# Optimization experiments

Hardware: AMD Instinct MI355X
Metric: run time of the kernel (lower is better)

Reference implementation:

```python
import jax, jax.numpy as jnp
import numpy as np

DIM = 768
HID = 3072  # 4 * DIM
EPS = 1e-5


def layer_norm(x, w, b):
    mu = jnp.mean(x, axis=-1, keepdims=True)
    var = jnp.var(x, axis=-1, keepdims=True)
    return (x - mu) * jax.lax.rsqrt(var + EPS) * w + b


def setup_inputs() -> dict:
    key = jax.random.key(0)
    ks = jax.random.split(key, 8)
    C, H = DIM, HID
    s = lambda fan_in: 1.0 / np.sqrt(fan_in)
    return {
        "x": jax.random.normal(ks[0], (32, 577, C), dtype=jnp.float32),
        "norm1_w": jnp.ones((C,), jnp.float32),
        "norm1_b": jnp.zeros((C,), jnp.float32),
        "qkv_w": jax.random.uniform(ks[1], (3 * C, C), jnp.float32, -s(C), s(C)),
        "proj_w": jax.random.uniform(ks[2], (C, C), jnp.float32, -s(C), s(C)),
        "proj_b": jax.random.uniform(ks[3], (C,), jnp.float32, -s(C), s(C)),
        "norm2_w": jnp.ones((C,), jnp.float32),
        "norm2_b": jnp.zeros((C,), jnp.float32),
        "fc1_w": jax.random.uniform(ks[4], (H, C), jnp.float32, -s(C), s(C)),
        "fc1_b": jax.random.uniform(ks[5], (H,), jnp.float32, -s(C), s(C)),
        "fc2_w": jax.random.uniform(ks[6], (C, H), jnp.float32, -s(H), s(H)),
        "fc2_b": jax.random.uniform(ks[7], (C,), jnp.float32, -s(H), s(H)),
    }


def reference(x, norm1_w, norm1_b, qkv_w, proj_w, proj_b,
              norm2_w, norm2_b, fc1_w, fc1_b, fc2_w, fc2_b):
    B, N, C = x.shape
    attn_size = int((N - 1) ** 0.5)
    scale = C ** -0.5

    # --- Attention on norm1(x) (single head) ---
    h = layer_norm(x, norm1_w, norm1_b)
    qkv = (h @ qkv_w.T).reshape(B, N, 3, C)           # [B,N,3,C]
    q, k, v = qkv[:, :, 0], qkv[:, :, 1], qkv[:, :, 2]
    attn = jax.nn.softmax(jnp.einsum('bnc,bmc->bnm', q, k) * scale, axis=-1)
    y = jnp.einsum('bnm,bmc->bnc', attn, v)           # [B,N,C]
    # Faithful to torch: .transpose(1,2).reshape(B,N,C) scrambles layout
    y = jnp.transpose(y, (0, 2, 1)).reshape(B, N, C)
    a = y @ proj_w.T + proj_b
    token_attn = attn[:, 0, 1:].reshape(B, 1, attn_size, attn_size)

    # Faithful to torch Block: input residual is discarded, attention out doubled
    x = a + a

    # --- MLP (exact GELU, as nn.GELU default) ---
    m = layer_norm(x, norm2_w, norm2_b)
    m = jax.nn.gelu(m @ fc1_w.T + fc1_b, approximate=False)
    m = m @ fc2_w.T + fc2_b
    x = x + m
    return (x, token_attn)
```

## Files before the change

### kernel.cpp

```cpp
#include <hip/hip_runtime.h>
#include <hip/hip_bf16.h>

#define Bz   32
#define Nn_  577
#define Np   640
#define Cc   768
#define Hh   3072
#define Mrows (Bz * Nn_)
#define OUT_X (Mrows * Cc)
#define SCALE 0.03608439182435161f

typedef unsigned short ushort_t;
typedef short short8 __attribute__((ext_vector_type(8)));
typedef float f32x4 __attribute__((ext_vector_type(4)));

__device__ __forceinline__ ushort_t f2b(float f) {
    __hip_bfloat16 h = __float2bfloat16(f);
    return *reinterpret_cast<ushort_t*>(&h);
}

__device__ __forceinline__ void gl16(const ushort_t* g, ushort_t* l) {
    __builtin_amdgcn_global_load_lds(
        (const __attribute__((address_space(1))) void*)g,
        (__attribute__((address_space(3))) void*)l, 16, 0, 0);
}

__device__ __forceinline__ float bsum(float v, float* sm) {
    #pragma unroll
    for (int o = 32; o > 0; o >>= 1) v += __shfl_down(v, o, 64);
    int lane = threadIdx.x & 63, wid = threadIdx.x >> 6;
    if (lane == 0) sm[wid] = v;
    __syncthreads();
    float r = sm[0] + sm[1] + sm[2] + sm[3];
    __syncthreads();
    return r;
}
__device__ __forceinline__ float bmax(float v, float* sm) {
    #pragma unroll
    for (int o = 32; o > 0; o >>= 1) v = fmaxf(v, __shfl_down(v, o, 64));
    int lane = threadIdx.x & 63, wid = threadIdx.x >> 6;
    if (lane == 0) sm[wid] = v;
    __syncthreads();
    float r = fmaxf(fmaxf(sm[0], sm[1]), fmaxf(sm[2], sm[3]));
    __syncthreads();
    return r;
}

__global__ void cvt_kernel(const float* __restrict__ in, ushort_t* __restrict__ out, int n) {
    int i = blockIdx.x * 256 + threadIdx.x;
    if (i < n) out[i] = f2b(in[i]);
}

__global__ void ln_bf16(const float* __restrict__ x, const float* __restrict__ w,
                        const float* __restrict__ b, ushort_t* __restrict__ out) {
    __shared__ float sm[8];
    long long row = blockIdx.x;
    const float* xr = x + row * Cc;
    float v[3]; float s = 0.f;
    #pragma unroll
    for (int i = 0; i < 3; ++i) { v[i] = xr[threadIdx.x + i * 256]; s += v[i]; }
    float mu = bsum(s, sm) * (1.f / (float)Cc);
    float sq = 0.f;
    #pragma unroll
    for (int i = 0; i < 3; ++i) { float d = v[i] - mu; sq += d * d; }
    float var = bsum(sq, sm + 4) * (1.f / (float)Cc);
    float inv = rsqrtf(var + 1e-5f);
    ushort_t* orow = out + row * Cc;
    #pragma unroll
    for (int i = 0; i < 3; ++i) {
        int c = threadIdx.x + i * 256;
        orow[c] = f2b((v[i] - mu) * inv * w[c] + b[c]);
    }
}

__global__ void softmax_bf16(const float* __restrict__ Sf, ushort_t* __restrict__ Sb,
                             float* __restrict__ tok) {
    __shared__ float sm[8];
    long long row = blockIdx.x;
    int b_l = (int)(row / Nn_), r = (int)(row - (long long)b_l * Nn_);
    const float* src = Sf + row * Np;
    ushort_t* dst = Sb + row * Np;
    float v[3]; float mx = -1e30f;
    #pragma unroll
    for (int i = 0; i < 3; ++i) {
        int c = threadIdx.x + i * 256;
        v[i] = (c < Nn_) ? src[c] : -1e30f;
        mx = fmaxf(mx, v[i]);
    }
    mx = bmax(mx, sm);
    float s = 0.f;
    #pragma unroll
    for (int i = 0; i < 3; ++i) {
        int c = threadIdx.x + i * 256;
        v[i] = (c < Nn_) ? expf(v[i] - mx) : 0.f;
        s += v[i];
    }
    s = bsum(s, sm + 4);
    float inv = 1.f / s;
    #pragma unroll
    for (int i = 0; i < 3; ++i) {
        int c = threadIdx.x + i * 256;
        float p = v[i] * inv;
        if (c < Np) dst[c] = (c < Nn_) ? f2b(p) : (ushort_t)0;
        if (r == 0 && c >= 1 && c < Nn_) tok[(long long)b_l * 576 + (c - 1)] = p;
    }
}

#define EPS_STORE  0
#define EPS_X2     1
#define EPS_GELU   2
#define EPS_ATOMIC 3
#define EPS_QKV    4

template<int EPI, typename OutT>
__global__ __launch_bounds__(256)
void mm_bf16(const ushort_t* __restrict__ A, long long sAb, int lda, int M,
             const ushort_t* __restrict__ B, long long sBb, int ldb, int Nv,
             const float* __restrict__ bias,
             OutT* __restrict__ O, long long sOb, int ldo,
             int K, float alpha,
             ushort_t* __restrict__ qQ, ushort_t* __restrict__ qK, ushort_t* __restrict__ qV)
{
    __shared__ __align__(16) ushort_t As[128 * 32];
    __shared__ __align__(16) ushort_t Bs[128 * 32];
    const int z = blockIdx.z;
    A += (long long)z * sAb; B += (long long)z * sBb;
    if (O) O += (long long)z * sOb;
    const int n0 = blockIdx.x * 128;
    const int m0 = blockIdx.y * 128;
    const int tid = threadIdx.x;
    const int lane = tid & 63;
    const int wv = tid >> 6;
    const int wr = (wv >> 1) << 6;
    const int wc = (wv & 1) << 6;
    const int fr = lane & 15;
    const int kq = lane >> 4;

    const int e0 = tid * 8, e1 = 2048 + tid * 8;
    const int ra0 = e0 >> 5, qa0 = (((e0 & 31) >> 3) ^ (ra0 & 3)) << 3;
    const int ra1 = e1 >> 5, qa1 = (((e1 & 31) >> 3) ^ (ra1 & 3)) << 3;
    const ushort_t* Ag0 = A + (long long)min(m0 + ra0, M - 1) * lda + qa0;
    const ushort_t* Ag1 = A + (long long)min(m0 + ra1, M - 1) * lda + qa1;
    const ushort_t* Bg0 = B + (long long)min(n0 + ra0, Nv - 1) * ldb + qa0;
    const ushort_t* Bg1 = B + (long long)min(n0 + ra1, Nv - 1) * ldb + qa1;

    f32x4 acc[4][4] = {};

    for (int k0 = 0; k0 < K; k0 += 32) {
        gl16(Ag0 + k0, &As[e0]);
        gl16(Ag1 + k0, &As[e1]);
        gl16(Bg0 + k0, &Bs[e0]);
        gl16(Bg1 + k0, &Bs[e1]);
        __syncthreads();
        short8 af[4], bfr[4];
        #pragma unroll
        for (int i = 0; i < 4; ++i) {
            int r = wr + i * 16 + fr;
            af[i] = *(const short8*)&As[r * 32 + ((kq ^ (r & 3)) << 3)];
        }
        #pragma unroll
        for (int j = 0; j < 4; ++j) {
            int r = wc + j * 16 + fr;
            bfr[j] = *(const short8*)&Bs[r * 32 + ((kq ^ (r & 3)) << 3)];
        }
        #pragma unroll
        for (int i = 0; i < 4; ++i)
            #pragma unroll
            for (int j = 0; j < 4; ++j)
                acc[i][j] = __builtin_amdgcn_mfma_f32_16x16x32_bf16(af[i], bfr[j], acc[i][j], 0, 0, 0);
        __syncthreads();
    }

    #pragma unroll
    for (int i = 0; i < 4; ++i) {
        int mb = m0 + wr + i * 16 + (lane >> 4) * 4;
        #pragma unroll
        for (int j = 0; j < 4; ++j) {
            int n = n0 + wc + j * 16 + fr;
            if (n >= Nv) continue;
            f32x4 v4 = acc[i][j];
            #pragma unroll
            for (int r = 0; r < 4; ++r) {
                int m = mb + r;
                if (m >= M) continue;
                float v = v4[r] * alpha;
                if constexpr (EPI == EPS_QKV) {
                    int b_l = m / Nn_, rr = m - b_l * Nn_;
                    if (n < Cc)            qQ[(long long)m * Cc + n] = f2b(v);
                    else if (n < 2 * Cc)   qK[(long long)m * Cc + (n - Cc)] = f2b(v);
                    else                   qV[((long long)b_l * Cc + (n - 2 * Cc)) * Np + rr] = f2b(v);
                } else if constexpr (EPI == EPS_ATOMIC) {
                    if (bias && z == 0) v += bias[n];
                    atomicAdd(&O[(long long)m * ldo + n], v);
                } else {
                    if (bias) v += bias[n];
                    if constexpr (EPI == EPS_X2) v *= 2.f;
                    if constexpr (EPI == EPS_GELU) v = 0.5f * v * (1.f + erff(v * 0.70710678118654752f));
                    long long oi = (long long)m * ldo + n;
                    if constexpr (sizeof(OutT) == 2) O[oi] = (OutT)f2b(v);
                    else                             O[oi] = (OutT)v;
                }
            }
        }
    }
}

extern "C" void kernel_launch(void* const* d_in, const int* in_sizes, int n_in,
                              void* d_out, int out_size, void* d_ws, size_t ws_size,
                              hipStream_t stream) {
    const float* x      = (const float*)d_in[0];
    const float* n1w    = (const float*)d_in[1];
    const float* n1b    = (const float*)d_in[2];
    const float* qkv_w  = (const float*)d_in[3];
    const float* proj_w = (const float*)d_in[4];
    const float* proj_b = (const float*)d_in[5];
    const float* n2w    = (const float*)d_in[6];
    const float* n2b    = (const float*)d_in[7];
    const float* fc1w   = (const float*)d_in[8];
    const float* fc1b   = (const float*)d_in[9];
    const float* fc2w   = (const float*)d_in[10];
    const float* fc2b   = (const float*)d_in[11];
    float* out = (float*)d_out;
    float* x2  = out;
    float* tok = out + OUT_X;

    char* ws = (char*)d_ws;
    const long long nWq = (long long)3 * Cc * Cc;
    const long long nWp = (long long)Cc * Cc;
    const long long nW1 = (long long)Hh * Cc;
    const long long nW2 = (long long)Cc * Hh;
    ushort_t* wq = (ushort_t*)ws;
    ushort_t* wp = wq + nWq;
    ushort_t* w1 = wp + nWp;
    ushort_t* w2 = w1 + nW1;
    const long long WBYTES = 2 * (nWq + nWp + nW1 + nW2);
    char* dyn = ws + WBYTES;
    long long avail = (long long)ws_size - WBYTES;

    const long long perG = 3LL * Nn_ * Cc * 2 + (long long)Cc * Np * 2
                         + (long long)Nn_ * Np * 4 + (long long)Nn_ * Np * 2;
    int G = 1;
    { const int o[6] = {32, 16, 8, 4, 2, 1};
      for (int i = 0; i < 6; ++i) if ((long long)o[i] * perG <= avail) { G = o[i]; break; } }
    int CH = Nn_;
    { const int o[6] = {32, 16, 8, 4, 2, 1};
      for (int i = 0; i < 6; ++i) if ((long long)o[i] * Nn_ * (Cc + Hh) * 2 <= avail) { CH = o[i] * Nn_; break; } }

    ushort_t* hbf = (ushort_t*)dyn;
    ushort_t* Q   = hbf + (long long)G * Nn_ * Cc;
    ushort_t* Kb  = Q   + (long long)G * Nn_ * Cc;
    ushort_t* Vt  = Kb  + (long long)G * Nn_ * Cc;
    float*    Sf  = (float*)(Vt + (long long)G * Cc * Np);
    ushort_t* Sb  = (ushort_t*)(Sf + (long long)G * Nn_ * Np);
    ushort_t* Yt  = hbf;
    ushort_t* g = (ushort_t*)dyn;
    ushort_t* t = g + (long long)CH * Cc;

    cvt_kernel<<<(int)((nWq + 255) / 256), 256, 0, stream>>>(qkv_w, wq, (int)nWq);
    cvt_kernel<<<(int)((nWp + 255) / 256), 256, 0, stream>>>(proj_w, wp, (int)nWp);
    cvt_kernel<<<(int)((nW1 + 255) / 256), 256, 0, stream>>>(fc1w, w1, (int)nW1);
    cvt_kernel<<<(int)((nW2 + 255) / 256), 256, 0, stream>>>(fc2w, w2, (int)nW2);

    for (int b0 = 0; b0 < Bz; b0 += G) {
        const int MR = G * Nn_;
        const int myM = (MR + 127) / 128;

        ln_bf16<<<MR, 256, 0, stream>>>(x + (long long)b0 * Nn_ * Cc, n1w, n1b, hbf);

        mm_bf16<EPS_QKV, float><<<dim3(18, myM, 1), 256, 0, stream>>>(
            hbf, 0, Cc, MR, wq, 0, Cc, 3 * Cc, nullptr,
            (float*)nullptr, 0, 0, Cc, 1.f, Q, Kb, Vt);

        mm_bf16<EPS_STORE, float><<<dim3(5, 5, G), 256, 0, stream>>>(
            Q, (long long)Nn_ * Cc, Cc, Nn_, Kb, (long long)Nn_ * Cc, Cc, Nn_, nullptr,
            Sf, (long long)Nn_ * Np, Np, Cc, SCALE, nullptr, nullptr, nullptr);

        softmax_bf16<<<MR, 256, 0, stream>>>(Sf, Sb, tok + (long long)b0 * 576);

        mm_bf16<EPS_STORE, ushort_t><<<dim3(5, 6, G), 256, 0, stream>>>(
            Vt, (long long)Cc * Np, Np, Cc, Sb, (long long)Nn_ * Np, Np, Nn_, nullptr,
            Yt, (long long)Cc * Nn_, Nn_, Np, 1.f, nullptr, nullptr, nullptr);

        mm_bf16<EPS_X2, float><<<dim3(6, myM, 1), 256, 0, stream>>>(
            Yt, 0, Cc, MR, wp, 0, Cc, Cc, proj_b,
            x2 + (long long)b0 * Nn_ * Cc, 0, Cc, Cc, 1.f, nullptr, nullptr, nullptr);
    }

    for (int c0 = 0; c0 < Mrows; c0 += CH) {
        const int cn = (Mrows - c0 < CH) ? (Mrows - c0) : CH;
        const int myC = (cn + 127) / 128;

        ln_bf16<<<cn, 256, 0, stream>>>(x2 + (long long)c0 * Cc, n2w, n2b, g);

        mm_bf16<EPS_GELU, ushort_t><<<dim3(24, myC, 1), 256, 0, stream>>>(
            g, 0, Cc, cn, w1, 0, Cc, Hh, fc1b,
            t, 0, Hh, Cc, 1.f, nullptr, nullptr, nullptr);

        mm_bf16<EPS_ATOMIC, float><<<dim3(6, myC, 2), 256, 0, stream>>>(
            t, Hh / 2, Hh, cn, w2, Hh / 2, Hh, Cc, fc2b,
            x2 + (long long)c0 * Cc, 0, Cc, Hh / 2, 1.f, nullptr, nullptr, nullptr);
    }
}
```

Baseline: 917.2 us.

## Double-buffer GEMM LDS tiles and replace split-K atomic fc2 with direct add

The bf16 MFMA GEMM now uses two LDS buffers, ping-ponged two K-tiles per loop iteration. The global-to-LDS load of the next tile is issued before the MFMAs on the current tile, so load latency can overlap compute. The fc2 GEMM no longer splits K into two z-slices with atomicAdd; one block covers the full K=3072 and does a plain read-add-store into the residual. This removes atomic traffic but halves the fc2 grid, and it doubles LDS use per block, which may reduce occupancy. The unrolled loop assumes an even tile count, which every K in use satisfies.

Measured after the change: 890.0 us. -3.0%, faster.

```diff
diff --git a/kernel.cpp b/kernel.cpp
--- a/kernel.cpp
+++ b/kernel.cpp
@@ -109,8 +109,35 @@
 #define EPS_STORE  0
 #define EPS_X2     1
 #define EPS_GELU   2
-#define EPS_ATOMIC 3
+#define EPS_ADD    3
 #define EPS_QKV    4
+
+#define MM_STAGE(AS, BS, k0) do {            \
+    gl16(Ag0 + (k0), &AS[e0]);               \
+    gl16(Ag1 + (k0), &AS[e1]);               \
+    gl16(Bg0 + (k0), &BS[e0]);               \
+    gl16(Bg1 + (k0), &BS[e1]);               \
+} while (0)
+
+#define MM_COMPUTE(AS, BS) do {                                             \
+    short8 af[4], bfr[4];                                                   \
+    _Pragma("unroll")                                                       \
+    for (int i = 0; i < 4; ++i) {                                           \
+        int r = wr + i * 16 + fr;                                           \
+        af[i] = *(const short8*)&AS[r * 32 + ((kq ^ (r & 3)) << 3)];        \
+    }                                                                       \
+    _Pragma("unroll")                                                       \
+    for (int j = 0; j < 4; ++j) {                                           \
+        int r = wc + j * 16 + fr;                                           \
+        bfr[j] = *(const short8*)&BS[r * 32 + ((kq ^ (r & 3)) << 3)];       \
+    }                                                                       \
+    _Pragma("unroll")                                                       \
+    for (int i = 0; i < 4; ++i)                                             \
+        _Pragma("unroll")                                                   \
+        for (int j = 0; j < 4; ++j)                                         \
+            acc[i][j] = __builtin_amdgcn_mfma_f32_16x16x32_bf16(            \
+                af[i], bfr[j], acc[i][j], 0, 0, 0);                         \
+} while (0)
 
 template<int EPI, typename OutT>
 __global__ __launch_bounds__(256)
@@ -121,8 +148,10 @@
              int K, float alpha,
              ushort_t* __restrict__ qQ, ushort_t* __restrict__ qK, ushort_t* __restrict__ qV)
 {
-    __shared__ __align__(16) ushort_t As[128 * 32];
-    __shared__ __align__(16) ushort_t Bs[128 * 32];
+    __shared__ __align__(16) ushort_t As0[128 * 32];
+    __shared__ __align__(16) ushort_t As1[128 * 32];
+    __shared__ __align__(16) ushort_t Bs0[128 * 32];
+    __shared__ __align__(16) ushort_t Bs1[128 * 32];
     const int z = blockIdx.z;
     A += (long long)z * sAb; B += (long long)z * sBb;
     if (O) O += (long long)z * sOb;
@@ -146,28 +175,17 @@
 
     f32x4 acc[4][4] = {};
 
-    for (int k0 = 0; k0 < K; k0 += 32) {
-        gl16(Ag0 + k0, &As[e0]);
-        gl16(Ag1 + k0, &As[e1]);
-        gl16(Bg0 + k0, &Bs[e0]);
-        gl16(Bg1 + k0, &Bs[e1]);
+    const int nt = K >> 5;
+
+    MM_STAGE(As0, Bs0, 0);
+    __syncthreads();
+
+    for (int t = 0; t < nt; t += 2) {
+        MM_STAGE(As1, Bs1, (t + 1) << 5);
+        MM_COMPUTE(As0, Bs0);
         __syncthreads();
-        short8 af[4], bfr[4];
-        #pragma unroll
-        for (int i = 0; i < 4; ++i) {
-            int r = wr + i * 16 + fr;
-            af[i] = *(const short8*)&As[r * 32 + ((kq ^ (r & 3)) << 3)];
-        }
-        #pragma unroll
-        for (int j = 0; j < 4; ++j) {
-            int r = wc + j * 16 + fr;
-            bfr[j] = *(const short8*)&Bs[r * 32 + ((kq ^ (r & 3)) << 3)];
-        }
-        #pragma unroll
-        for (int i = 0; i < 4; ++i)
-            #pragma unroll
-            for (int j = 0; j < 4; ++j)
-                acc[i][j] = __builtin_amdgcn_mfma_f32_16x16x32_bf16(af[i], bfr[j], acc[i][j], 0, 0, 0);
+        if (t + 2 < nt) MM_STAGE(As0, Bs0, (t + 2) << 5);
+        MM_COMPUTE(As1, Bs1);
         __syncthreads();
     }
 
@@ -189,9 +207,10 @@
                     if (n < Cc)            qQ[(long long)m * Cc + n] = f2b(v);
                     else if (n < 2 * Cc)   qK[(long long)m * Cc + (n - Cc)] = f2b(v);
                     else                   qV[((long long)b_l * Cc + (n - 2 * Cc)) * Np + rr] = f2b(v);
-                } else if constexpr (EPI == EPS_ATOMIC) {
-                    if (bias && z == 0) v += bias[n];
-                    atomicAdd(&O[(long long)m * ldo + n], v);
+                } else if constexpr (EPI == EPS_ADD) {
+                    if (bias) v += bias[n];
+                    long long oi = (long long)m * ldo + n;
+                    O[oi] += v;
                 } else {
                     if (bias) v += bias[n];
                     if constexpr (EPI == EPS_X2) v *= 2.f;
@@ -296,8 +315,8 @@
             g, 0, Cc, cn, w1, 0, Cc, Hh, fc1b,
             t, 0, Hh, Cc, 1.f, nullptr, nullptr, nullptr);
 
-        mm_bf16<EPS_ATOMIC, float><<<dim3(6, myC, 2), 256, 0, stream>>>(
-            t, Hh / 2, Hh, cn, w2, Hh / 2, Hh, Cc, fc2b,
-            x2 + (long long)c0 * Cc, 0, Cc, Hh / 2, 1.f, nullptr, nullptr, nullptr);
-    }
-}
+        mm_bf16<EPS_ADD, float><<<dim3(6, myC, 1), 256, 0, stream>>>(
+            t, 0, Hh, cn, w2, 0, Hh, Cc, fc2b,
+            x2 + (long long)c0 * Cc, 0, Cc, Hh, 1.f, nullptr, nullptr, nullptr);
+    }
+}
```
